# Kernel optimization log

Hardware: AMD Instinct MI355X
Metric: run time of the kernel (lower is better)

## Reference

```python
import jax, jax.numpy as jnp
import numpy as np

N = 100000
E = 1600000
IN_C, HID_C, OUT_C = 128, 64, 64


def setup_inputs() -> dict:
    key = jax.random.key(0)
    k1, k2, k3, k4, k5 = jax.random.split(key, 5)
    x = jax.random.normal(k1, (N, IN_C), dtype=jnp.float32)
    edge_index = jax.random.randint(k2, (2, E), 0, N, dtype=jnp.int64)
    # Glorot-style params per GCNConv (weight [in,out], bias [out])
    W1 = jax.random.normal(k3, (IN_C, HID_C), dtype=jnp.float32) / np.sqrt(IN_C)
    b1 = jnp.zeros((HID_C,), dtype=jnp.float32)
    W2 = jax.random.normal(k4, (HID_C, OUT_C), dtype=jnp.float32) / np.sqrt(HID_C)
    b2 = jnp.zeros((OUT_C,), dtype=jnp.float32)
    return {"x": x, "edge_index": edge_index, "W1": W1, "b1": b1, "W2": W2, "b2": b2}


def _gcn_norm(edge_index, n):
    # add self-loops, then symmetric normalization deg^{-1/2} A deg^{-1/2}
    loop = jnp.arange(n, dtype=edge_index.dtype)
    src = jnp.concatenate([edge_index[0], loop])
    dst = jnp.concatenate([edge_index[1], loop])
    deg = jax.ops.segment_sum(jnp.ones_like(dst, dtype=jnp.float32), dst, num_segments=n)
    dinv = jnp.where(deg > 0, jax.lax.rsqrt(deg), 0.0)
    norm = dinv[src] * dinv[dst]  # [E+N]
    return src, dst, norm


def _gcn_conv(x, W, b, src, dst, norm, n):
    h = x @ W                                   # [N, out]
    m = h[src] * norm[:, None]                  # gather + scale  [E+N, out]
    out = jax.ops.segment_sum(m, dst, num_segments=n)  # scatter-add at dst
    return out + b


def reference(x, edge_index, W1, b1, W2, b2):
    n = x.shape[0]
    src, dst, norm = _gcn_norm(edge_index, n)
    h = jax.nn.relu(_gcn_conv(x, W1, b1, src, dst, norm, n))
    out = _gcn_conv(h, W2, b2, src, dst, norm, n)
    return out
```

## Files before the change

### kernel.cpp

```cpp
#include <hip/hip_runtime.h>
#include <hip/hip_fp16.h>


#define CAP   64
#define CAPB  3072
#define BKMAX 1024

typedef _Float16 f16x8 __attribute__((ext_vector_type(8)));
typedef float f32x4 __attribute__((ext_vector_type(4)));

struct alignas(8) H4 { __half2 a, b; };
__device__ inline H4 pack4(float x, float y, float z, float w) {
  H4 r; r.a = __floats2half2_rn(x, y); r.b = __floats2half2_rn(z, w); return r;
}

__global__ void detect_i64_kernel(const unsigned int* __restrict__ w, int ncheck,
                                  int* __restrict__ flag) {
  __shared__ int nz;
  if (threadIdx.x == 0) nz = 0;
  __syncthreads();
  for (int i = threadIdx.x; i < ncheck; i += blockDim.x) {
    if (w[2 * i + 1] != 0u) nz = 1;
  }
  __syncthreads();
  if (threadIdx.x == 0) flag[0] = (nz == 0) ? 1 : 0;
}

__global__ __launch_bounds__(256) void hist_gemm_kernel(
    const int* __restrict__ edges, int E, const int* __restrict__ flag,
    int* __restrict__ Hh, int SB, int nbk,
    int* __restrict__ tmp_pk, int* __restrict__ tmp_mt,
    const float* __restrict__ A, const float* __restrict__ W,
    __half* __restrict__ g, int n) {
  __shared__ __align__(16) char smem[34816];
  const int t = threadIdx.x;
  const int bid = (int)blockIdx.x;

  if (bid < SB) {
    int* hist = (int*)smem;
    const int f = flag[0];
    const int blk0 = bid * 2048;

    for (int i = t; i < nbk; i += 256) hist[i] = 0;
    __syncthreads();

    if (blk0 + 2048 <= E) {
      int sv[8], dv[8];
      if (f) {
#pragma unroll
        for (int u = 0; u < 4; ++u) {
          const int eg = blk0 + (u * 256 + t) * 2;
          const int4 a = *(const int4*)&edges[2 * (size_t)eg];
          const int4 b = *(const int4*)&edges[2 * ((size_t)E + eg)];
          sv[u * 2] = a.x; sv[u * 2 + 1] = a.z;
          dv[u * 2] = b.x; dv[u * 2 + 1] = b.z;
        }
      } else {
#pragma unroll
        for (int u = 0; u < 2; ++u) {
          const int eg = blk0 + (u * 256 + t) * 4;
          const int4 a = *(const int4*)&edges[eg];
          const int4 b = *(const int4*)&edges[(size_t)E + eg];
          sv[u * 4] = a.x; sv[u * 4 + 1] = a.y; sv[u * 4 + 2] = a.z; sv[u * 4 + 3] = a.w;
          dv[u * 4] = b.x; dv[u * 4 + 1] = b.y; dv[u * 4 + 2] = b.z; dv[u * 4 + 3] = b.w;
        }
      }
      int pk[8], mt[8];
#pragma unroll
      for (int i = 0; i < 8; ++i) {
        const int bk = dv[i] >> 7;
        const int rk = atomicAdd(&hist[bk], 1);
        pk[i] = ((dv[i] & 127) << 17) | sv[i];
        mt[i] = bk | (rk << 10);
      }
      if (f) {
#pragma unroll
        for (int u = 0; u < 4; ++u) {
          const int eg = blk0 + (u * 256 + t) * 2;
          *(int2*)&tmp_pk[eg] = make_int2(pk[u * 2], pk[u * 2 + 1]);
          *(int2*)&tmp_mt[eg] = make_int2(mt[u * 2], mt[u * 2 + 1]);
        }
      } else {
        *(int4*)&tmp_pk[blk0 + t * 4]        = make_int4(pk[0], pk[1], pk[2], pk[3]);
        *(int4*)&tmp_pk[blk0 + 1024 + t * 4] = make_int4(pk[4], pk[5], pk[6], pk[7]);
        *(int4*)&tmp_mt[blk0 + t * 4]        = make_int4(mt[0], mt[1], mt[2], mt[3]);
        *(int4*)&tmp_mt[blk0 + 1024 + t * 4] = make_int4(mt[4], mt[5], mt[6], mt[7]);
      }
    } else {
      for (int e = blk0 + t; e < E; e += 256) {
        const int s = f ? edges[2 * (size_t)e] : edges[e];
        const int d = f ? edges[2 * ((size_t)E + e)] : edges[(size_t)E + e];
        const int bk = d >> 7;
        const int rk = atomicAdd(&hist[bk], 1);
        tmp_pk[e] = ((d & 127) << 17) | s;
        tmp_mt[e] = bk | (rk << 10);
      }
    }
    __syncthreads();
    for (int i = t; i < nbk; i += 256) Hh[(size_t)i * SB + bid] = hist[i];
    return;
  }

  _Float16 (*Af)[136] = (_Float16(*)[136])smem;
  _Float16 (*Wf)[136] = (_Float16(*)[136])(smem + 17408);
  const int row0 = (bid - SB) * 64;

  {
    const int r = t >> 2, k0 = (t & 3) << 5;
    const int gr = row0 + r;
    if (gr < n) {
#pragma unroll
      for (int q = 0; q < 4; ++q) {
        float4 a = *(const float4*)&A[(size_t)gr * 128 + k0 + q * 8];
        float4 b = *(const float4*)&A[(size_t)gr * 128 + k0 + q * 8 + 4];
        f16x8 v;
        v[0] = (_Float16)a.x; v[1] = (_Float16)a.y; v[2] = (_Float16)a.z; v[3] = (_Float16)a.w;
        v[4] = (_Float16)b.x; v[5] = (_Float16)b.y; v[6] = (_Float16)b.z; v[7] = (_Float16)b.w;
        *(f16x8*)&Af[r][k0 + q * 8] = v;
      }
    } else {
      f16x8 z = {0, 0, 0, 0, 0, 0, 0, 0};
#pragma unroll
      for (int q = 0; q < 4; ++q) *(f16x8*)&Af[r][k0 + q * 8] = z;
    }
  }
  {
    const int c = t & 63, kq = t >> 6;
#pragma unroll
    for (int i = 0; i < 32; ++i)
      Wf[c][kq * 32 + i] = (_Float16)W[(size_t)(kq * 32 + i) * 64 + c];
  }
  __syncthreads();

  const int wid = t >> 6, lane = t & 63;
  const int lr = lane & 15, kg = lane >> 4;
  f32x4 acc[4] = {{0, 0, 0, 0}, {0, 0, 0, 0}, {0, 0, 0, 0}, {0, 0, 0, 0}};
#pragma unroll
  for (int kc = 0; kc < 4; ++kc) {
    f16x8 av = *(const f16x8*)&Af[wid * 16 + lr][kc * 32 + kg * 8];
#pragma unroll
    for (int ct = 0; ct < 4; ++ct) {
      f16x8 bv = *(const f16x8*)&Wf[ct * 16 + lr][kc * 32 + kg * 8];
      acc[ct] = __builtin_amdgcn_mfma_f32_16x16x32_f16(av, bv, acc[ct], 0, 0, 0);
    }
  }
#pragma unroll
  for (int ct = 0; ct < 4; ++ct) {
#pragma unroll
    for (int rg = 0; rg < 4; ++rg) {
      const int r = row0 + wid * 16 + kg * 4 + rg;
      if (r < n) g[(size_t)r * 64 + ct * 16 + lr] = (__half)(float)acc[ct][rg];
    }
  }
}

__global__ __launch_bounds__(256) void scan_hist_kernel(
    int* __restrict__ Hh, int SB, int* __restrict__ T) {
  __shared__ int sm[256];
  __shared__ int carry;
  const int b = blockIdx.x;
  const int t = threadIdx.x;
  if (t == 0) carry = 0;
  __syncthreads();
  int* __restrict__ row = Hh + (size_t)b * SB;
  for (int base = 0; base < SB; base += 256) {
    const int i = base + t;
    const int v = (i < SB) ? row[i] : 0;
    sm[t] = v;
    __syncthreads();
    for (int off = 1; off < 256; off <<= 1) {
      int u = (t >= off) ? sm[t - off] : 0;
      __syncthreads();
      sm[t] += u;
      __syncthreads();
    }
    const int excl = sm[t] - v + carry;
    if (i < SB) row[i] = excl;
    __syncthreads();
    if (t == 0) carry += sm[255];
    __syncthreads();
  }
  if (t == 0) T[b] = carry;
}

__global__ __launch_bounds__(256) void place_kernel(
    const int* __restrict__ tmp_pk, const int* __restrict__ tmp_mt,
    const int* __restrict__ Hh, int SB, int E, int* __restrict__ arena) {
  const int e0 = ((int)blockIdx.x * 256 + (int)threadIdx.x) * 4;
  if (e0 >= E) return;
  const int blk = e0 >> 11;
  if (e0 + 4 <= E) {
    const int4 pk = *(const int4*)&tmp_pk[e0];
    const int4 mt = *(const int4*)&tmp_mt[e0];
    const int b0 = mt.x & 1023, b1 = mt.y & 1023, b2 = mt.z & 1023, b3 = mt.w & 1023;
    const int p0 = Hh[(size_t)b0 * SB + blk] + (mt.x >> 10);
    const int p1 = Hh[(size_t)b1 * SB + blk] + (mt.y >> 10);
    const int p2 = Hh[(size_t)b2 * SB + blk] + (mt.z >> 10);
    const int p3 = Hh[(size_t)b3 * SB + blk] + (mt.w >> 10);
    if (p0 < CAPB) arena[(size_t)b0 * CAPB + p0] = pk.x;
    if (p1 < CAPB) arena[(size_t)b1 * CAPB + p1] = pk.y;
    if (p2 < CAPB) arena[(size_t)b2 * CAPB + p2] = pk.z;
    if (p3 < CAPB) arena[(size_t)b3 * CAPB + p3] = pk.w;
  } else {
    for (int e = e0; e < E; ++e) {
      const int mt = tmp_mt[e];
      const int bk = mt & 1023;
      const int p = Hh[(size_t)bk * SB + blk] + (mt >> 10);
      if (p < CAPB) arena[(size_t)bk * CAPB + p] = tmp_pk[e];
    }
  }
}

__global__ __launch_bounds__(512) void cluster_csr_kernel(
    const int* __restrict__ T, const int* __restrict__ arena,
    int n, int* __restrict__ counts, float* __restrict__ dinv,
    int* __restrict__ csrp) {
  __shared__ int lc[128];
  const int b = blockIdx.x;
  const int t = threadIdx.x;
  if (t < 128) lc[t] = 0;
  __syncthreads();
  int cnt = T[b];
  if (cnt > CAPB) cnt = CAPB;
  const int* __restrict__ seg = &arena[(size_t)b * CAPB];
  for (int j = t; j < cnt; j += 512) {
    const int p = seg[j];
    const int dl = p >> 17;
    const int s = p & 131071;
    const int r = atomicAdd(&lc[dl], 1);
    if (r < CAP) csrp[((size_t)(b << 7) + dl) * CAP + r] = s;
  }
  __syncthreads();
  const int d = (b << 7) + t;
  if (t < 128 && d < n) {
    counts[d] = lc[t];
    dinv[d] = rsqrtf((float)(lc[t] + 1));
  }
}

__global__ __launch_bounds__(256) void gemm2_kernel(
    const _Float16* __restrict__ h, const float* __restrict__ W,
    const float* __restrict__ dinv, __half* __restrict__ out, int n) {
  __shared__ __align__(16) _Float16 Af[64][72];
  __shared__ __align__(16) _Float16 Wf[64][72];
  const int t = threadIdx.x;
  const int row0 = blockIdx.x * 64;

  {
    const int r = t >> 2, k0 = (t & 3) << 4;
    const int gr = row0 + r;
    if (gr < n) {
      *(f16x8*)&Af[r][k0] = *(const f16x8*)&h[(size_t)gr * 64 + k0];
      *(f16x8*)&Af[r][k0 + 8] = *(const f16x8*)&h[(size_t)gr * 64 + k0 + 8];
    } else {
      f16x8 z = {0, 0, 0, 0, 0, 0, 0, 0};
      *(f16x8*)&Af[r][k0] = z;
      *(f16x8*)&Af[r][k0 + 8] = z;
    }
  }
  {
    const int c = t & 63, kq = t >> 6;
#pragma unroll
    for (int i = 0; i < 16; ++i)
      Wf[c][kq * 16 + i] = (_Float16)W[(size_t)(kq * 16 + i) * 64 + c];
  }
  __syncthreads();

  const int wid = t >> 6, lane = t & 63;
  const int lr = lane & 15, kg = lane >> 4;
  f32x4 acc[4] = {{0, 0, 0, 0}, {0, 0, 0, 0}, {0, 0, 0, 0}, {0, 0, 0, 0}};
#pragma unroll
  for (int kc = 0; kc < 2; ++kc) {
    f16x8 av = *(const f16x8*)&Af[wid * 16 + lr][kc * 32 + kg * 8];
#pragma unroll
    for (int ct = 0; ct < 4; ++ct) {
      f16x8 bv = *(const f16x8*)&Wf[ct * 16 + lr][kc * 32 + kg * 8];
      acc[ct] = __builtin_amdgcn_mfma_f32_16x16x32_f16(av, bv, acc[ct], 0, 0, 0);
    }
  }
  float sc[4];
#pragma unroll
  for (int rg = 0; rg < 4; ++rg) {
    const int r = row0 + wid * 16 + kg * 4 + rg;
    sc[rg] = (r < n) ? dinv[r] : 0.f;
  }
#pragma unroll
  for (int ct = 0; ct < 4; ++ct) {
#pragma unroll
    for (int rg = 0; rg < 4; ++rg) {
      const int r = row0 + wid * 16 + kg * 4 + rg;
      if (r < n) out[(size_t)r * 64 + ct * 16 + lr] = (__half)((float)acc[ct][rg] * sc[rg]);
    }
  }
}

template <bool EDGE_SCALE, bool RELU, typename OUT>
__global__ __launch_bounds__(256) void agg_kernel(
    const __half* __restrict__ hs, const int* __restrict__ counts,
    const int* __restrict__ csrp, const float* __restrict__ dinv,
    const float* __restrict__ bias, OUT* __restrict__ out, int n) {
  const int wid = blockIdx.x * 4 + ((int)threadIdx.x >> 6);
  if (wid * 4 >= n) return;
  const int lane = (int)threadIdx.x & 63;
  const int q = lane >> 4;
  const int ql = lane & 15;
  const int d = wid * 4 + q;
  const bool active = d < n;
  const int dc = active ? d : n - 1;

  int len = counts[dc];
  if (len > CAP) len = CAP;
  if (!active) len = 0;
  const int* __restrict__ row = &csrp[(size_t)dc * CAP];
  const float dd = dinv[dc];

  H4 sv = *(const H4*)&hs[(size_t)dc * 64 + (ql << 2)];
  float2 s01 = __half22float2(sv.a), s23 = __half22float2(sv.b);
  const float ws = EDGE_SCALE ? dd : 1.f;
  float a0 = ws * s01.x, a1 = ws * s01.y, a2 = ws * s23.x, a3 = ws * s23.y;

  for (int j = 0; __any(j < len); j += 8) {
    int sidx[8];
    bool pr[8];
#pragma unroll
    for (int u = 0; u < 8; ++u) {
      pr[u] = (j + u) < len;
      sidx[u] = pr[u] ? row[j + u] : dc;
    }
    H4 v[8];
#pragma unroll
    for (int u = 0; u < 8; ++u) v[u] = *(const H4*)&hs[(size_t)sidx[u] * 64 + (ql << 2)];
#pragma unroll
    for (int u = 0; u < 8; ++u) {
      float w = pr[u] ? (EDGE_SCALE ? dinv[sidx[u]] : 1.f) : 0.f;
      float2 f = __half22float2(v[u].a), g = __half22float2(v[u].b);
      a0 = fmaf(w, f.x, a0); a1 = fmaf(w, f.y, a1);
      a2 = fmaf(w, g.x, a2); a3 = fmaf(w, g.y, a3);
    }
  }

  if (active) {
    const float4 b4 = *(const float4*)&bias[ql << 2];
    float4 o;
    o.x = fmaf(a0, dd, b4.x); o.y = fmaf(a1, dd, b4.y);
    o.z = fmaf(a2, dd, b4.z); o.w = fmaf(a3, dd, b4.w);
    if (RELU) {
      o.x = fmaxf(o.x, 0.f); o.y = fmaxf(o.y, 0.f);
      o.z = fmaxf(o.z, 0.f); o.w = fmaxf(o.w, 0.f);
    }
    if constexpr (sizeof(OUT) == 2) {
      *(H4*)&out[(size_t)d * 64 + (ql << 2)] = pack4(o.x, o.y, o.z, o.w);
    } else {
      *(float4*)&out[(size_t)d * 64 + (ql << 2)] = o;
    }
  }
}

extern "C" void kernel_launch(void* const* d_in, const int* in_sizes, int n_in,
                              void* d_out, int out_size, void* d_ws, size_t ws_size,
                              hipStream_t stream) {
  const float* x  = (const float*)d_in[0];
  const int*   ei = (const int*)d_in[1];
  const float* W1 = (const float*)d_in[2];
  const float* b1 = (const float*)d_in[3];
  const float* W2 = (const float*)d_in[4];
  const float* b2 = (const float*)d_in[5];
  float* out = (float*)d_out;

  const int N = in_sizes[0] / 128;
  const int E = in_sizes[1] / 2;
  const int NBK = (N + 127) >> 7;
  const int SB = (E + 2047) / 2048;
  const int G1 = (N + 63) / 64;

  char* ws = (char*)d_ws;
  size_t off = 0;
  auto take = [&](size_t bytes) -> void* {
    void* p = ws + off;
    off += (bytes + 255) & ~(size_t)255;
    return p;
  };
  int*    flag   = (int*)take(sizeof(int));
  int*    Hh     = (int*)take((size_t)NBK * SB * 4);
  int*    T      = (int*)take((size_t)NBK * 4);
  int*    counts = (int*)take((size_t)N * 4);
  float*  dinv   = (float*)take((size_t)N * 4);
  int*    tmp_pk = (int*)take((size_t)E * 4);
  int*    tmp_mt = (int*)take((size_t)E * 4);
  int*    arena  = (int*)take((size_t)NBK * CAPB * 4);
  int*    csrp   = (int*)take((size_t)N * CAP * 4);
  __half* hsf    = (__half*)take((size_t)N * 64 * 2);
  __half* hh     = (__half*)take((size_t)N * 64 * 2);
  (void)ws_size; (void)n_in; (void)out_size;

  detect_i64_kernel<<<1, 256, 0, stream>>>((const unsigned int*)ei, 4096, flag);

  hist_gemm_kernel<<<SB + G1, 256, 0, stream>>>(
      ei, E, flag, Hh, SB, NBK, tmp_pk, tmp_mt, x, W1, hsf, N);

  scan_hist_kernel<<<NBK, 256, 0, stream>>>(Hh, SB, T);

  place_kernel<<<((E + 3) / 4 + 255) / 256, 256, 0, stream>>>(
      tmp_pk, tmp_mt, Hh, SB, E, arena);

  cluster_csr_kernel<<<NBK, 512, 0, stream>>>(T, arena, N, counts, dinv, csrp);

  agg_kernel<true, true, __half><<<(N + 15) / 16, 256, 0, stream>>>(
      hsf, counts, csrp, dinv, b1, hh, N);

  gemm2_kernel<<<G1, 256, 0, stream>>>((const _Float16*)hh, W2, dinv, hsf, N);

  agg_kernel<false, false, float><<<(N + 15) / 16, 256, 0, stream>>>(
      hsf, counts, csrp, dinv, b2, out, N);
}
```

Measured before the change: 154.1 us.

## Sort destination nodes by degree to balance aggregation wavefronts

Adds a counting sort (histogram, scan, place) of nodes by in-degree to build a permutation, and both aggregation kernels now process nodes in that order, writing outputs to the permuted index. Grouping four nodes with similar degree per wavefront cuts divergence from the any-lane loop bound. In exchange it adds three small kernel launches, a single-block serial scan, and an extra indirection that scatters the writes and the self-feature reads.

```diff
diff --git a/kernel.cpp b/kernel.cpp
--- a/kernel.cpp
+++ b/kernel.cpp
@@ -5,6 +5,7 @@
 #define CAP   64
 #define CAPB  3072
 #define BKMAX 1024
+#define DBIN  65
 
 typedef _Float16 f16x8 __attribute__((ext_vector_type(8)));
 typedef float f32x4 __attribute__((ext_vector_type(4)));
@@ -238,6 +239,63 @@
   }
 }
 
+
+__global__ __launch_bounds__(256) void perm_hist_kernel(
+    const int* __restrict__ counts, int n, int* __restrict__ Hp, int PB) {
+  __shared__ int hist[DBIN];
+  const int t = threadIdx.x;
+  const int blk0 = (int)blockIdx.x * 2048;
+  if (t < DBIN) hist[t] = 0;
+  __syncthreads();
+  for (int i = blk0 + t; i < blk0 + 2048 && i < n; i += 256) {
+    int dg = counts[i];
+    if (dg > 64) dg = 64;
+    atomicAdd(&hist[dg], 1);
+  }
+  __syncthreads();
+  if (t < DBIN) Hp[(size_t)t * PB + blockIdx.x] = hist[t];
+}
+
+__global__ __launch_bounds__(256) void perm_scan_kernel(int* __restrict__ Hp, int len) {
+  __shared__ int sm[256];
+  __shared__ int carry;
+  const int t = threadIdx.x;
+  if (t == 0) carry = 0;
+  __syncthreads();
+  for (int base = 0; base < len; base += 256) {
+    const int i = base + t;
+    const int v = (i < len) ? Hp[i] : 0;
+    sm[t] = v;
+    __syncthreads();
+    for (int off = 1; off < 256; off <<= 1) {
+      int u = (t >= off) ? sm[t - off] : 0;
+      __syncthreads();
+      sm[t] += u;
+      __syncthreads();
+    }
+    if (i < len) Hp[i] = sm[t] - v + carry;
+    __syncthreads();
+    if (t == 0) carry += sm[255];
+    __syncthreads();
+  }
+}
+
+__global__ __launch_bounds__(256) void perm_place_kernel(
+    const int* __restrict__ counts, int n, const int* __restrict__ Hp, int PB,
+    int* __restrict__ perm) {
+  __shared__ int hist[DBIN];
+  const int t = threadIdx.x;
+  const int blk0 = (int)blockIdx.x * 2048;
+  if (t < DBIN) hist[t] = 0;
+  __syncthreads();
+  for (int i = blk0 + t; i < blk0 + 2048 && i < n; i += 256) {
+    int dg = counts[i];
+    if (dg > 64) dg = 64;
+    const int rk = atomicAdd(&hist[dg], 1);
+    perm[Hp[(size_t)dg * PB + blockIdx.x] + rk] = i;
+  }
+}
+
 __global__ __launch_bounds__(256) void gemm2_kernel(
     const _Float16* __restrict__ h, const float* __restrict__ W,
     const float* __restrict__ dinv, __half* __restrict__ out, int n) {
@@ -298,15 +356,16 @@
 __global__ __launch_bounds__(256) void agg_kernel(
     const __half* __restrict__ hs, const int* __restrict__ counts,
     const int* __restrict__ csrp, const float* __restrict__ dinv,
-    const float* __restrict__ bias, OUT* __restrict__ out, int n) {
+    const float* __restrict__ bias, const int* __restrict__ perm,
+    OUT* __restrict__ out, int n) {
   const int wid = blockIdx.x * 4 + ((int)threadIdx.x >> 6);
   if (wid * 4 >= n) return;
   const int lane = (int)threadIdx.x & 63;
   const int q = lane >> 4;
   const int ql = lane & 15;
-  const int d = wid * 4 + q;
-  const bool active = d < n;
-  const int dc = active ? d : n - 1;
+  const int idx = wid * 4 + q;
+  const bool active = idx < n;
+  const int dc = perm[active ? idx : n - 1];
 
   int len = counts[dc];
   if (len > CAP) len = CAP;
@@ -349,9 +408,9 @@
       o.z = fmaxf(o.z, 0.f); o.w = fmaxf(o.w, 0.f);
     }
     if constexpr (sizeof(OUT) == 2) {
-      *(H4*)&out[(size_t)d * 64 + (ql << 2)] = pack4(o.x, o.y, o.z, o.w);
+      *(H4*)&out[(size_t)dc * 64 + (ql << 2)] = pack4(o.x, o.y, o.z, o.w);
     } else {
-      *(float4*)&out[(size_t)d * 64 + (ql << 2)] = o;
+      *(float4*)&out[(size_t)dc * 64 + (ql << 2)] = o;
     }
   }
 }
@@ -372,6 +431,7 @@
   const int NBK = (N + 127) >> 7;
   const int SB = (E + 2047) / 2048;
   const int G1 = (N + 63) / 64;
+  const int PB = (N + 2047) / 2048;
 
   char* ws = (char*)d_ws;
   size_t off = 0;
@@ -385,6 +445,8 @@
   int*    T      = (int*)take((size_t)NBK * 4);
   int*    counts = (int*)take((size_t)N * 4);
   float*  dinv   = (float*)take((size_t)N * 4);
+  int*    Hp     = (int*)take((size_t)DBIN * PB * 4);
+  int*    perm   = (int*)take((size_t)N * 4);
   int*    tmp_pk = (int*)take((size_t)E * 4);
   int*    tmp_mt = (int*)take((size_t)E * 4);
   int*    arena  = (int*)take((size_t)NBK * CAPB * 4);
@@ -405,11 +467,15 @@
 
   cluster_csr_kernel<<<NBK, 512, 0, stream>>>(T, arena, N, counts, dinv, csrp);
 
+  perm_hist_kernel<<<PB, 256, 0, stream>>>(counts, N, Hp, PB);
+  perm_scan_kernel<<<1, 256, 0, stream>>>(Hp, DBIN * PB);
+  perm_place_kernel<<<PB, 256, 0, stream>>>(counts, N, Hp, PB, perm);
+
   agg_kernel<true, true, __half><<<(N + 15) / 16, 256, 0, stream>>>(
-      hsf, counts, csrp, dinv, b1, hh, N);
+      hsf, counts, csrp, dinv, b1, perm, hh, N);
 
   gemm2_kernel<<<G1, 256, 0, stream>>>((const _Float16*)hh, W2, dinv, hsf, N);
 
   agg_kernel<false, false, float><<<(N + 15) / 16, 256, 0, stream>>>(
-      hsf, counts, csrp, dinv, b2, out, N);
-}
+      hsf, counts, csrp, dinv, b2, perm, out, N);
+}
```

Measured after the change: 179.3 us. 1.16x slower.
